# Performance work log

Measured on AMD Instinct MI355X. Metric: run time of the kernel, lower is better.

The kernel has to match this reference:

```python
import jax, jax.numpy as jnp
import numpy as np

U1, U2 = 128, 32  # GRU units


def gru(x, kernel, rec_kernel, bias, act, rec_act):
    """Keras GRU with reset_after=True. x: [B,T,F], kernel: [F,3U],
    rec_kernel: [U,3U], bias: [2,3U] (input bias, recurrent bias).
    Gate order is [z, r, h]. Returns (sequence [B,T,U], last state [B,U])."""
    B = x.shape[0]
    U = rec_kernel.shape[0]
    # Precompute the input projection for all timesteps in one big matmul.
    xb = jnp.einsum('btf,fg->btg', x, kernel) + bias[0]  # [B,T,3U]

    def step(h, xt):
        inner = h @ rec_kernel + bias[1]                 # [B,3U]
        xz, xr, xh = jnp.split(xt, 3, axis=-1)
        iz, ir, ih = jnp.split(inner, 3, axis=-1)
        z = rec_act(xz + iz)
        r = rec_act(xr + ir)
        hh = act(xh + r * ih)
        h_new = z * h + (1.0 - z) * hh
        return h_new, h_new

    h0 = jnp.zeros((B, U), x.dtype)
    hT, hs = jax.lax.scan(step, h0, jnp.swapaxes(xb, 0, 1))  # scan over T
    return jnp.swapaxes(hs, 0, 1), hT


def setup_inputs() -> dict:
    key = jax.random.key(0)
    ks = jax.random.split(key, 9)
    B, T, F = 512, 1024, 1
    s = 0.05
    return {
        'x':   jax.random.normal(ks[0], (B, T, F), jnp.float32),
        'k1':  jax.random.normal(ks[1], (F, 3 * U1), jnp.float32) * s,
        'rk1': jax.random.normal(ks[2], (U1, 3 * U1), jnp.float32) * s,
        'b1':  jnp.zeros((2, 3 * U1), jnp.float32),
        'k2':  jax.random.normal(ks[3], (U1, 3 * U2), jnp.float32) * s,
        'rk2': jax.random.normal(ks[4], (U2, 3 * U2), jnp.float32) * s,
        'b2':  jnp.zeros((2, 3 * U2), jnp.float32),
        'wd':  jax.random.normal(ks[5], (U2, 1), jnp.float32) * s,
        'bd':  jnp.zeros((1,), jnp.float32),
    }


def reference(x, k1, rk1, b1, k2, rk2, b2, wd, bd):
    # GRU-1: activation=tanh, recurrent_activation=relu, return_sequences=True
    seq1, _ = gru(x, k1, rk1, b1, jnp.tanh, jax.nn.relu)
    # Dropout(0.5) is identity at inference time.
    # GRU-2: activation=relu, recurrent_activation=sigmoid, return last state
    _, h2 = gru(seq1, k2, rk2, b2, jax.nn.relu, jax.nn.sigmoid)
    return h2 @ wd + bd  # [B,1]
```

## Files before the change

### kernel.cpp

```cpp
#include <hip/hip_runtime.h>
#include <math.h>

#define TT 1024
#define U1 128
#define U2 32
#define NCOL 480
#define NQ 120
#define NUQ 4

__device__ __forceinline__ float fast_tanh(float v) {
    float e = __expf(2.f * v);
    return 1.f - 2.f / (e + 1.f);
}
__device__ __forceinline__ float fast_sig(float v) {
    return 1.f / (1.f + __expf(-v));
}

__global__ __launch_bounds__(512, 1)
void gru_stack_kernel(const float* __restrict__ x,
                      const float* __restrict__ k1,
                      const float* __restrict__ rk1,
                      const float* __restrict__ b1,
                      const float* __restrict__ k2,
                      const float* __restrict__ rk2,
                      const float* __restrict__ b2,
                      const float* __restrict__ wd,
                      const float* __restrict__ bd,
                      float* __restrict__ out)
{
    __shared__ __align__(16) float h1s[2][U1];
    __shared__ __align__(16) float h2s[2][U2];
    __shared__ __align__(16) float part1[2][NUQ][NCOL];
    __shared__ __align__(16) float part2[2][96];

    const int t  = threadIdx.x;
    const int b0 = blockIdx.x * 2;

    if (t < 2 * U1) ((float*)h1s)[t] = 0.f;
    if (t < 2 * U2) ((float*)h2s)[t] = 0.f;

    float4 w4[32];
    const float4* pb0 = nullptr;
    const float4* pb1 = nullptr;
    float4* pd0 = nullptr;
    float4* pd1 = nullptr;
    const bool is_dot = (t < 504);
    if (t < 480) {
        const int uq = t / NQ, q = t % NQ;
        const int c0 = 4 * q, ub = 32 * uq;
#pragma unroll
        for (int j = 0; j < 32; ++j) {
            const int u = ub + j;
            float vv[4];
#pragma unroll
            for (int r = 0; r < 4; ++r) {
                const int c = c0 + r;
                vv[r] = (c < 384) ? rk1[u * 384 + c] : k2[u * 96 + (c - 384)];
            }
            w4[j] = make_float4(vv[0], vv[1], vv[2], vv[3]);
        }
        pb0 = (const float4*)&h1s[0][ub];
        pb1 = (const float4*)&h1s[1][ub];
        pd0 = (float4*)&part1[0][uq][c0];
        pd1 = (float4*)&part1[1][uq][c0];
    } else if (t < 504) {
        const int q2 = t - 480, c0 = 4 * q2;
#pragma unroll
        for (int j = 0; j < 32; ++j)
            w4[j] = make_float4(rk2[j * 96 + c0 + 0], rk2[j * 96 + c0 + 1],
                                rk2[j * 96 + c0 + 2], rk2[j * 96 + c0 + 3]);
        pb0 = (const float4*)&h2s[0][0];
        pb1 = (const float4*)&h2s[1][0];
        pd0 = (float4*)&part2[0][c0];
        pd1 = (float4*)&part2[1][c0];
    }

    const int ju = t & 127, bu = t >> 7;
    float k1z = 0, k1r = 0, k1h = 0, bz = 0, br = 0, bhx = 0, bhr = 0, h_old = 0;
    if (t < 256) {
        k1z = k1[ju]; k1r = k1[128 + ju]; k1h = k1[256 + ju];
        bz  = b1[ju]       + b1[384 + ju];
        br  = b1[128 + ju] + b1[384 + 128 + ju];
        bhx = b1[256 + ju];
        bhr = b1[384 + 256 + ju];
    }
    const int tau = t - 256, j2 = tau & 31, bb2 = tau >> 5;
    float bz2 = 0, br2 = 0, bh2x = 0, bh2r = 0, h2_old = 0;
    if (t >= 256 && t < 320) {
        bz2  = b2[j2]      + b2[96 + j2];
        br2  = b2[32 + j2] + b2[96 + 32 + j2];
        bh2x = b2[64 + j2];
        bh2r = b2[96 + 64 + j2];
    }

    __syncthreads();

    for (int i = 0; i <= TT; ++i) {
        float xv = 0.f;
        if (t < 256 && i < TT) xv = x[(b0 + bu) * TT + i];

        if (is_dot) {
            float4 a0 = make_float4(0.f, 0.f, 0.f, 0.f);
            float4 a1 = make_float4(0.f, 0.f, 0.f, 0.f);
#pragma unroll
            for (int j4 = 0; j4 < 8; ++j4) {
                float4 hv0 = pb0[j4];
                float4 hv1 = pb1[j4];
                float ha0[4] = {hv0.x, hv0.y, hv0.z, hv0.w};
                float ha1[4] = {hv1.x, hv1.y, hv1.z, hv1.w};
#pragma unroll
                for (int e = 0; e < 4; ++e) {
                    const float4 wv = w4[4 * j4 + e];
                    const float he0 = ha0[e], he1 = ha1[e];
                    a0.x = fmaf(he0, wv.x, a0.x);
                    a0.y = fmaf(he0, wv.y, a0.y);
                    a0.z = fmaf(he0, wv.z, a0.z);
                    a0.w = fmaf(he0, wv.w, a0.w);
                    a1.x = fmaf(he1, wv.x, a1.x);
                    a1.y = fmaf(he1, wv.y, a1.y);
                    a1.z = fmaf(he1, wv.z, a1.z);
                    a1.w = fmaf(he1, wv.w, a1.w);
                }
            }
            *pd0 = a0;
            *pd1 = a1;
        }
        __syncthreads();

        if (t < 256 && i < TT) {
            float iz = part1[bu][0][ju] + part1[bu][1][ju]
                     + part1[bu][2][ju] + part1[bu][3][ju];
            float ir = part1[bu][0][128 + ju] + part1[bu][1][128 + ju]
                     + part1[bu][2][128 + ju] + part1[bu][3][128 + ju];
            float ih = part1[bu][0][256 + ju] + part1[bu][1][256 + ju]
                     + part1[bu][2][256 + ju] + part1[bu][3][256 + ju];
            float z  = fmaxf(fmaf(xv, k1z, bz) + iz, 0.f);
            float r  = fmaxf(fmaf(xv, k1r, br) + ir, 0.f);
            float hh = fast_tanh(fmaf(xv, k1h, bhx) + r * (ih + bhr));
            h_old = fmaf(z, h_old - hh, hh);
            h1s[bu][ju] = h_old;
        } else if (t >= 256 && t < 320 && i >= 1) {
            float xz = part1[bb2][0][384 + j2] + part1[bb2][1][384 + j2]
                     + part1[bb2][2][384 + j2] + part1[bb2][3][384 + j2];
            float xr = part1[bb2][0][416 + j2] + part1[bb2][1][416 + j2]
                     + part1[bb2][2][416 + j2] + part1[bb2][3][416 + j2];
            float xh = part1[bb2][0][448 + j2] + part1[bb2][1][448 + j2]
                     + part1[bb2][2][448 + j2] + part1[bb2][3][448 + j2];
            float iz = part2[bb2][j2];
            float ir = part2[bb2][32 + j2];
            float ih = part2[bb2][64 + j2];
            float z  = fast_sig(xz + iz + bz2);
            float r  = fast_sig(xr + ir + br2);
            float hh = fmaxf(xh + bh2x + r * (ih + bh2r), 0.f);
            h2_old = fmaf(z, h2_old - hh, hh);
            h2s[bb2][j2] = h2_old;
        }
        __syncthreads();
    }

    if (t < 64) {
        const int b = t >> 5, j = t & 31;
        float p = h2s[b][j] * wd[j];
#pragma unroll
        for (int m = 16; m >= 1; m >>= 1) p += __shfl_xor(p, m, 64);
        if (j == 0) out[b0 + b] = p + bd[0];
    }
}

extern "C" void kernel_launch(void* const* d_in, const int* in_sizes, int n_in,
                              void* d_out, int out_size, void* d_ws, size_t ws_size,
                              hipStream_t stream) {
    const float* x   = (const float*)d_in[0];
    const float* k1  = (const float*)d_in[1];
    const float* rk1 = (const float*)d_in[2];
    const float* b1  = (const float*)d_in[3];
    const float* k2  = (const float*)d_in[4];
    const float* rk2 = (const float*)d_in[5];
    const float* b2  = (const float*)d_in[6];
    const float* wd  = (const float*)d_in[7];
    const float* bd  = (const float*)d_in[8];
    float* out = (float*)d_out;

    dim3 grid(256), block(512);
    hipLaunchKernelGGL(gru_stack_kernel, grid, block, 0, stream,
                       x, k1, rk1, b1, k2, rk2, b2, wd, bd, out);
}
```

Measured before the change: 1.186 ms.

## Ping-pong two batch rows across phases to overlap matvec with gate updates

Restructures the time loop into 2T+3 phases. Each phase computes the recurrent matvec for one batch row while a separate group of threads (t 320-479) does the gate update for the other row, so only one barrier is needed per phase instead of two per step. It also stages the whole x sequence for both rows in shared memory up front, which removes a global load per step. The cost is twice as many loop iterations, each doing half the FMA work, and an extra 8 KB of shared memory.

```diff
diff --git a/kernel.cpp b/kernel.cpp
--- a/kernel.cpp
+++ b/kernel.cpp
@@ -32,12 +32,15 @@
     __shared__ __align__(16) float h2s[2][U2];
     __shared__ __align__(16) float part1[2][NUQ][NCOL];
     __shared__ __align__(16) float part2[2][96];
+    __shared__ __align__(16) float xs[2][TT];
 
     const int t  = threadIdx.x;
     const int b0 = blockIdx.x * 2;
 
     if (t < 2 * U1) ((float*)h1s)[t] = 0.f;
     if (t < 2 * U2) ((float*)h2s)[t] = 0.f;
+    for (int idx = t; idx < 2 * TT; idx += 512)
+        ((float*)xs)[idx] = x[b0 * TT + idx];
 
     float4 w4[32];
     const float4* pb0 = nullptr;
@@ -75,18 +78,22 @@
         pd1 = (float4*)&part2[1][c0];
     }
 
-    const int ju = t & 127, bu = t >> 7;
-    float k1z = 0, k1r = 0, k1h = 0, bz = 0, br = 0, bhx = 0, bhr = 0, h_old = 0;
-    if (t < 256) {
+    const int ju = t - 320;
+    const bool isU1 = (t >= 320 && t < 448);
+    float k1z = 0, k1r = 0, k1h = 0, bz = 0, br = 0, bhx = 0, bhr = 0;
+    float hoA = 0.f, hoB = 0.f;
+    if (isU1) {
         k1z = k1[ju]; k1r = k1[128 + ju]; k1h = k1[256 + ju];
         bz  = b1[ju]       + b1[384 + ju];
         br  = b1[128 + ju] + b1[384 + 128 + ju];
         bhx = b1[256 + ju];
         bhr = b1[384 + 256 + ju];
     }
-    const int tau = t - 256, j2 = tau & 31, bb2 = tau >> 5;
-    float bz2 = 0, br2 = 0, bh2x = 0, bh2r = 0, h2_old = 0;
-    if (t >= 256 && t < 320) {
+    const int j2 = t - 448;
+    const bool isU2 = (t >= 448 && t < 480);
+    float bz2 = 0, br2 = 0, bh2x = 0, bh2r = 0;
+    float h2oA = 0.f, h2oB = 0.f;
+    if (isU2) {
         bz2  = b2[j2]      + b2[96 + j2];
         br2  = b2[32 + j2] + b2[96 + 32 + j2];
         bh2x = b2[64 + j2];
@@ -95,65 +102,73 @@
 
     __syncthreads();
 
-    for (int i = 0; i <= TT; ++i) {
-        float xv = 0.f;
-        if (t < 256 && i < TT) xv = x[(b0 + bu) * TT + i];
-
-        if (is_dot) {
-            float4 a0 = make_float4(0.f, 0.f, 0.f, 0.f);
-            float4 a1 = make_float4(0.f, 0.f, 0.f, 0.f);
+    for (int p = 0; p <= 2 * TT + 2; ++p) {
+        const int X = p & 1, Y = 1 - X;
+        const int i_dot = p >> 1;
+        const int i_u   = (p - 1) >> 1;
+        const bool doU1 = isU1 && (p >= 1) && (i_u < TT);
+        const bool doU2 = isU2 && (i_u >= 1);
+
+        float e_xv = 0, e_iz = 0, e_ir = 0, e_ih = 0;
+        if (doU1) {
+            e_xv = xs[Y][i_u];
+            e_iz = part1[Y][0][ju] + part1[Y][1][ju]
+                 + part1[Y][2][ju] + part1[Y][3][ju];
+            e_ir = part1[Y][0][128 + ju] + part1[Y][1][128 + ju]
+                 + part1[Y][2][128 + ju] + part1[Y][3][128 + ju];
+            e_ih = part1[Y][0][256 + ju] + part1[Y][1][256 + ju]
+                 + part1[Y][2][256 + ju] + part1[Y][3][256 + ju];
+        }
+        float g_xz = 0, g_xr = 0, g_xh = 0, g_iz = 0, g_ir = 0, g_ih = 0;
+        if (doU2) {
+            g_xz = part1[Y][0][384 + j2] + part1[Y][1][384 + j2]
+                 + part1[Y][2][384 + j2] + part1[Y][3][384 + j2];
+            g_xr = part1[Y][0][416 + j2] + part1[Y][1][416 + j2]
+                 + part1[Y][2][416 + j2] + part1[Y][3][416 + j2];
+            g_xh = part1[Y][0][448 + j2] + part1[Y][1][448 + j2]
+                 + part1[Y][2][448 + j2] + part1[Y][3][448 + j2];
+            g_iz = part2[Y][j2];
+            g_ir = part2[Y][32 + j2];
+            g_ih = part2[Y][64 + j2];
+        }
+
+        if (is_dot && i_dot <= TT) {
+            const float4* pb = X ? pb1 : pb0;
+            float4 a = make_float4(0.f, 0.f, 0.f, 0.f);
 #pragma unroll
             for (int j4 = 0; j4 < 8; ++j4) {
-                float4 hv0 = pb0[j4];
-                float4 hv1 = pb1[j4];
-                float ha0[4] = {hv0.x, hv0.y, hv0.z, hv0.w};
-                float ha1[4] = {hv1.x, hv1.y, hv1.z, hv1.w};
+                float4 hv = pb[j4];
+                float ha[4] = {hv.x, hv.y, hv.z, hv.w};
 #pragma unroll
                 for (int e = 0; e < 4; ++e) {
                     const float4 wv = w4[4 * j4 + e];
-                    const float he0 = ha0[e], he1 = ha1[e];
-                    a0.x = fmaf(he0, wv.x, a0.x);
-                    a0.y = fmaf(he0, wv.y, a0.y);
-                    a0.z = fmaf(he0, wv.z, a0.z);
-                    a0.w = fmaf(he0, wv.w, a0.w);
-                    a1.x = fmaf(he1, wv.x, a1.x);
-                    a1.y = fmaf(he1, wv.y, a1.y);
-                    a1.z = fmaf(he1, wv.z, a1.z);
-                    a1.w = fmaf(he1, wv.w, a1.w);
+                    const float he = ha[e];
+                    a.x = fmaf(he, wv.x, a.x);
+                    a.y = fmaf(he, wv.y, a.y);
+                    a.z = fmaf(he, wv.z, a.z);
+                    a.w = fmaf(he, wv.w, a.w);
                 }
             }
-            *pd0 = a0;
-            *pd1 = a1;
-        }
-        __syncthreads();
-
-        if (t < 256 && i < TT) {
-            float iz = part1[bu][0][ju] + part1[bu][1][ju]
-                     + part1[bu][2][ju] + part1[bu][3][ju];
-            float ir = part1[bu][0][128 + ju] + part1[bu][1][128 + ju]
-                     + part1[bu][2][128 + ju] + part1[bu][3][128 + ju];
-            float ih = part1[bu][0][256 + ju] + part1[bu][1][256 + ju]
-                     + part1[bu][2][256 + ju] + part1[bu][3][256 + ju];
-            float z  = fmaxf(fmaf(xv, k1z, bz) + iz, 0.f);
-            float r  = fmaxf(fmaf(xv, k1r, br) + ir, 0.f);
-            float hh = fast_tanh(fmaf(xv, k1h, bhx) + r * (ih + bhr));
-            h_old = fmaf(z, h_old - hh, hh);
-            h1s[bu][ju] = h_old;
-        } else if (t >= 256 && t < 320 && i >= 1) {
-            float xz = part1[bb2][0][384 + j2] + part1[bb2][1][384 + j2]
-                     + part1[bb2][2][384 + j2] + part1[bb2][3][384 + j2];
-            float xr = part1[bb2][0][416 + j2] + part1[bb2][1][416 + j2]
-                     + part1[bb2][2][416 + j2] + part1[bb2][3][416 + j2];
-            float xh = part1[bb2][0][448 + j2] + part1[bb2][1][448 + j2]
-                     + part1[bb2][2][448 + j2] + part1[bb2][3][448 + j2];
-            float iz = part2[bb2][j2];
-            float ir = part2[bb2][32 + j2];
-            float ih = part2[bb2][64 + j2];
-            float z  = fast_sig(xz + iz + bz2);
-            float r  = fast_sig(xr + ir + br2);
-            float hh = fmaxf(xh + bh2x + r * (ih + bh2r), 0.f);
-            h2_old = fmaf(z, h2_old - hh, hh);
-            h2s[bb2][j2] = h2_old;
+            *(X ? pd1 : pd0) = a;
+        }
+
+        if (doU1) {
+            float z  = fmaxf(fmaf(e_xv, k1z, bz) + e_iz, 0.f);
+            float r  = fmaxf(fmaf(e_xv, k1r, br) + e_ir, 0.f);
+            float hh = fast_tanh(fmaf(e_xv, k1h, bhx) + r * (e_ih + bhr));
+            float ho = Y ? hoB : hoA;
+            float hn = fmaf(z, ho - hh, hh);
+            if (Y) hoB = hn; else hoA = hn;
+            h1s[Y][ju] = hn;
+        }
+        if (doU2) {
+            float z  = fast_sig(g_xz + g_iz + bz2);
+            float r  = fast_sig(g_xr + g_ir + br2);
+            float hh = fmaxf(g_xh + bh2x + r * (g_ih + bh2r), 0.f);
+            float ho = Y ? h2oB : h2oA;
+            float hn = fmaf(z, ho - hh, hh);
+            if (Y) h2oB = hn; else h2oA = hn;
+            h2s[Y][j2] = hn;
         }
         __syncthreads();
     }
```

New measurement: 1.407 ms. 18.6% more time.

## Use packed FP32 FMA in recurrent dot products and preload inputs into LDS

Applied to the files above, without the earlier changes.

Rewrites the per-step recurrent matvec so it uses v_pk_fma_f32 inline asm, which computes two output columns per instruction with op_sel broadcasting one hidden-state element. This halves the FMA instruction count on the critical path. It also stages the whole input sequence for both batch rows into shared memory up front, removing a global load on each timestep. The inline asm limits compiler scheduling and may add register pressure from the f2 weight arrays.

```diff
diff --git a/kernel.cpp b/kernel.cpp
--- a/kernel.cpp
+++ b/kernel.cpp
@@ -7,6 +7,13 @@
 #define NCOL 480
 #define NQ 120
 #define NUQ 4
+
+typedef float f2 __attribute__((ext_vector_type(2)));
+
+#define PK_LO(acc, w, h) asm("v_pk_fma_f32 %0, %1, %2, %0 op_sel:[0,0,0] op_sel_hi:[1,0,1]" \
+                             : "+v"(acc) : "v"(w), "v"(h))
+#define PK_HI(acc, w, h) asm("v_pk_fma_f32 %0, %1, %2, %0 op_sel:[0,1,0] op_sel_hi:[1,1,1]" \
+                             : "+v"(acc) : "v"(w), "v"(h))
 
 __device__ __forceinline__ float fast_tanh(float v) {
     float e = __expf(2.f * v);
@@ -32,16 +39,19 @@
     __shared__ __align__(16) float h2s[2][U2];
     __shared__ __align__(16) float part1[2][NUQ][NCOL];
     __shared__ __align__(16) float part2[2][96];
+    __shared__ __align__(16) float xs[2][TT];
 
     const int t  = threadIdx.x;
     const int b0 = blockIdx.x * 2;
 
     if (t < 2 * U1) ((float*)h1s)[t] = 0.f;
     if (t < 2 * U2) ((float*)h2s)[t] = 0.f;
+    for (int idx = t; idx < 2 * TT; idx += 512)
+        ((float*)xs)[idx] = x[b0 * TT + idx];
 
-    float4 w4[32];
-    const float4* pb0 = nullptr;
-    const float4* pb1 = nullptr;
+    f2 wA[32], wB[32];
+    const f2* pb0 = nullptr;
+    const f2* pb1 = nullptr;
     float4* pd0 = nullptr;
     float4* pd1 = nullptr;
     const bool is_dot = (t < 504);
@@ -57,20 +67,22 @@
                 const int c = c0 + r;
                 vv[r] = (c < 384) ? rk1[u * 384 + c] : k2[u * 96 + (c - 384)];
             }
-            w4[j] = make_float4(vv[0], vv[1], vv[2], vv[3]);
+            wA[j].x = vv[0]; wA[j].y = vv[1];
+            wB[j].x = vv[2]; wB[j].y = vv[3];
         }
-        pb0 = (const float4*)&h1s[0][ub];
-        pb1 = (const float4*)&h1s[1][ub];
+        pb0 = (const f2*)&h1s[0][ub];
+        pb1 = (const f2*)&h1s[1][ub];
         pd0 = (float4*)&part1[0][uq][c0];
         pd1 = (float4*)&part1[1][uq][c0];
     } else if (t < 504) {
         const int q2 = t - 480, c0 = 4 * q2;
 #pragma unroll
-        for (int j = 0; j < 32; ++j)
-            w4[j] = make_float4(rk2[j * 96 + c0 + 0], rk2[j * 96 + c0 + 1],
-                                rk2[j * 96 + c0 + 2], rk2[j * 96 + c0 + 3]);
-        pb0 = (const float4*)&h2s[0][0];
-        pb1 = (const float4*)&h2s[1][0];
+        for (int j = 0; j < 32; ++j) {
+            wA[j].x = rk2[j * 96 + c0 + 0]; wA[j].y = rk2[j * 96 + c0 + 1];
+            wB[j].x = rk2[j * 96 + c0 + 2]; wB[j].y = rk2[j * 96 + c0 + 3];
+        }
+        pb0 = (const f2*)&h2s[0][0];
+        pb1 = (const f2*)&h2s[1][0];
         pd0 = (float4*)&part2[0][c0];
         pd1 = (float4*)&part2[1][c0];
     }
@@ -96,38 +108,29 @@
     __syncthreads();
 
     for (int i = 0; i <= TT; ++i) {
-        float xv = 0.f;
-        if (t < 256 && i < TT) xv = x[(b0 + bu) * TT + i];
-
         if (is_dot) {
-            float4 a0 = make_float4(0.f, 0.f, 0.f, 0.f);
-            float4 a1 = make_float4(0.f, 0.f, 0.f, 0.f);
+            f2 aA0 = {0.f, 0.f}, aB0 = {0.f, 0.f};
+            f2 aA1 = {0.f, 0.f}, aB1 = {0.f, 0.f};
 #pragma unroll
-            for (int j4 = 0; j4 < 8; ++j4) {
-                float4 hv0 = pb0[j4];
-                float4 hv1 = pb1[j4];
-                float ha0[4] = {hv0.x, hv0.y, hv0.z, hv0.w};
-                float ha1[4] = {hv1.x, hv1.y, hv1.z, hv1.w};
-#pragma unroll
-                for (int e = 0; e < 4; ++e) {
-                    const float4 wv = w4[4 * j4 + e];
-                    const float he0 = ha0[e], he1 = ha1[e];
-                    a0.x = fmaf(he0, wv.x, a0.x);
-                    a0.y = fmaf(he0, wv.y, a0.y);
-                    a0.z = fmaf(he0, wv.z, a0.z);
-                    a0.w = fmaf(he0, wv.w, a0.w);
-                    a1.x = fmaf(he1, wv.x, a1.x);
-                    a1.y = fmaf(he1, wv.y, a1.y);
-                    a1.z = fmaf(he1, wv.z, a1.z);
-                    a1.w = fmaf(he1, wv.w, a1.w);
-                }
+            for (int k = 0; k < 16; ++k) {
+                const f2 h0 = pb0[k];
+                const f2 h1 = pb1[k];
+                PK_LO(aA0, wA[2 * k],     h0);
+                PK_HI(aA0, wA[2 * k + 1], h0);
+                PK_LO(aB0, wB[2 * k],     h0);
+                PK_HI(aB0, wB[2 * k + 1], h0);
+                PK_LO(aA1, wA[2 * k],     h1);
+                PK_HI(aA1, wA[2 * k + 1], h1);
+                PK_LO(aB1, wB[2 * k],     h1);
+                PK_HI(aB1, wB[2 * k + 1], h1);
             }
-            *pd0 = a0;
-            *pd1 = a1;
+            *pd0 = make_float4(aA0.x, aA0.y, aB0.x, aB0.y);
+            *pd1 = make_float4(aA1.x, aA1.y, aB1.x, aB1.y);
         }
         __syncthreads();
 
         if (t < 256 && i < TT) {
+            const float xv = xs[bu][i];
             float iz = part1[bu][0][ju] + part1[bu][1][ju]
                      + part1[bu][2][ju] + part1[bu][3][ju];
             float ir = part1[bu][0][128 + ju] + part1[bu][1][128 + ju]
```

Measured after the change: 1.140 ms. -3.9%, faster.
